# Kernel optimization log

Hardware: AMD Instinct MI355X
Metric: run time of the kernel (lower is better)

The kernel has to match this reference:

```python
import jax, jax.numpy as jnp
import numpy as np

N_IN, N_OUT = 1152, 10          # input/output capsule counts
D_IN, D_OUT = 8, 16             # input/output capsule dims
NUM_ROUTING = 3
BATCH = 256
EPS = 1e-9


def squash(s, axis=-1):
    # squash(s) = (|s|^2 / (1 + |s|^2)) * s / |s|
    sq = jnp.sum(s * s, axis=axis, keepdims=True)
    return (sq / (1.0 + sq)) * s / jnp.sqrt(sq + EPS)


def setup_inputs() -> dict:
    key = jax.random.key(0)
    kx, kw = jax.random.split(key)
    x = jax.random.normal(kx, (BATCH, D_IN, N_IN), dtype=jnp.float32)
    weight = jax.random.normal(kw, (N_IN, N_OUT, D_OUT, D_IN), dtype=jnp.float32)
    return {"x": x, "weight": weight}


def reference(x, weight):
    # u_hat[b,i,j,:] = W[i,j] @ x[b,:,i]   -> [B, N_IN, N_OUT, D_OUT]
    u_hat = jnp.einsum('ijod,bdi->bijo', weight, x)
    # routing logits b_ij shared across the batch (fully bipartite capsule graph)
    b = jnp.zeros((N_IN, N_OUT), dtype=x.dtype)
    v = None
    for _ in range(NUM_ROUTING):
        c = jax.nn.softmax(b, axis=1)                       # coupling over output caps j
        s = jnp.einsum('ij,bijo->bjo', c, u_hat)            # weighted sum of predictions
        v = squash(s)                                       # [B, N_OUT, D_OUT]
        # agreement: <u_hat, v>, averaged over batch (as in the DGL example)
        b = b + jnp.mean(jnp.einsum('bijo,bjo->bij', u_hat, v), axis=0)
    return v
```

## Files before the change

kernel.cpp:

```cpp
#include <hip/hip_runtime.h>

#define B_     256
#define NI_    1152
#define NO_    10
#define DO_    16
#define DI_    8
#define PAIRS_ 160
#define SEGS_  128
#define ISEG_  (NI_/SEGS_)
#define PP_    5
#define SC_    4


__global__ __launch_bounds__(256) void prep_kernel(const float* __restrict__ x,
                                                   float* __restrict__ xT,
                                                   float* __restrict__ blog,
                                                   float* __restrict__ cmat)
{
    int g = blockIdx.x * 256 + threadIdx.x;
    int b = g & 255;
    int r = g >> 8;
    int d = r & 7;
    int i = r >> 3;
    xT[g] = x[(size_t)b * (NI_ * DI_) + d * NI_ + i];
    if (g < NI_ * NO_) { blog[g] = 0.f; cmat[g] = 0.1f; }
}

__global__ __launch_bounds__(256) void sv_kernel(const float* __restrict__ xT,
                                                 const float* __restrict__ W,
                                                 const float* __restrict__ cmat,
                                                 float* __restrict__ partial)
{
    __shared__ __align__(16) float xs[2][DI_ * B_];
    int ps   = blockIdx.x;
    int seg  = blockIdx.y;
    int tid  = threadIdx.x;
    int lane = tid & 63;
    int pg   = __builtin_amdgcn_readfirstlane(tid >> 6);
    int p0   = ps * (4 * PP_) + pg * PP_;
    int b0   = lane * 4;
    int i0   = seg * ISEG_;

    float acc[PP_][4];
#pragma unroll
    for (int p = 0; p < PP_; ++p)
#pragma unroll
        for (int r = 0; r < 4; ++r) acc[p][r] = 0.f;

    float4 nx0, nx1;
    {
        const float4* src = (const float4*)(xT + (size_t)i0 * (DI_ * B_));
        nx0 = src[tid * 2];
        nx1 = src[tid * 2 + 1];
    }
    int buf = 0;
    for (int ii = 0; ii < ISEG_; ++ii) {
        int i = i0 + ii;
        ((float4*)xs[buf])[tid * 2]     = nx0;
        ((float4*)xs[buf])[tid * 2 + 1] = nx1;
        __syncthreads();
        if (ii + 1 < ISEG_) {
            const float4* src = (const float4*)(xT + (size_t)(i + 1) * (DI_ * B_));
            nx0 = src[tid * 2];
            nx1 = src[tid * 2 + 1];
        }
        float xv[DI_][4];
#pragma unroll
        for (int d = 0; d < DI_; ++d) {
            float4 t4 = *(const float4*)&xs[buf][d * B_ + b0];
            xv[d][0] = t4.x; xv[d][1] = t4.y; xv[d][2] = t4.z; xv[d][3] = t4.w;
        }
        const float* __restrict__ crow = cmat + i * NO_;
        const float* __restrict__ wb = W + (size_t)(i * PAIRS_ + p0) * DI_;
#pragma unroll
        for (int p = 0; p < PP_; ++p) {
            const float* wr = wb + p * DI_;
            float cv = crow[(p0 + p) >> 4];
#pragma unroll
            for (int r = 0; r < 4; ++r) {
                float u = wr[0] * xv[0][r] + wr[1] * xv[1][r]
                        + wr[2] * xv[2][r] + wr[3] * xv[3][r]
                        + wr[4] * xv[4][r] + wr[5] * xv[5][r]
                        + wr[6] * xv[6][r] + wr[7] * xv[7][r];
                acc[p][r] = fmaf(cv, u, acc[p][r]);
            }
        }
        buf ^= 1;
    }
#pragma unroll
    for (int p = 0; p < PP_; ++p) {
        float4 o4 = make_float4(acc[p][0], acc[p][1], acc[p][2], acc[p][3]);
        *(float4*)&partial[(size_t)(seg * PAIRS_ + p0 + p) * B_ + b0] = o4;
    }
}

__global__ __launch_bounds__(256) void red1_kernel(const float* __restrict__ partial,
                                                   float* __restrict__ part2)
{
    int pair = blockIdx.x;
    int sc   = blockIdx.y;
    int b    = threadIdx.x;
    float s = 0.f;
    for (int k = 0; k < SEGS_ / SC_; ++k) {
        int seg = sc * (SEGS_ / SC_) + k;
        s += partial[(size_t)(seg * PAIRS_ + pair) * B_ + b];
    }
    part2[((size_t)sc * PAIRS_ + pair) * B_ + b] = s;
}

__global__ __launch_bounds__(256) void red2_kernel(const float* __restrict__ part2,
                                                   float* __restrict__ vbuf,
                                                   float* __restrict__ out,
                                                   int write_out)
{
    int j    = blockIdx.x;
    int bq   = blockIdx.y;
    int lane = threadIdx.x & 63;
    int og   = threadIdx.x >> 6;
    int b    = bq * 64 + lane;
    __shared__ float so[DO_][64];
#pragma unroll
    for (int oo = 0; oo < 4; ++oo) {
        int o = og * 4 + oo;
        int pair = j * DO_ + o;
        float s = part2[((size_t)0 * PAIRS_ + pair) * B_ + b]
                + part2[((size_t)1 * PAIRS_ + pair) * B_ + b]
                + part2[((size_t)2 * PAIRS_ + pair) * B_ + b]
                + part2[((size_t)3 * PAIRS_ + pair) * B_ + b];
        so[o][lane] = s;
    }
    __syncthreads();
    float sq = 0.f;
#pragma unroll
    for (int o = 0; o < DO_; ++o) sq += so[o][lane] * so[o][lane];
    float f = (sq / (1.f + sq)) * rsqrtf(sq + 1e-9f);
#pragma unroll
    for (int oo = 0; oo < 4; ++oo) {
        int o = og * 4 + oo;
        float vv = so[o][lane] * f;
        vbuf[(j * DO_ + o) * B_ + b] = vv;
        if (write_out) out[(size_t)b * PAIRS_ + j * DO_ + o] = vv;
    }
}

__global__ __launch_bounds__(256) void agree_kernel(const float* __restrict__ xT,
                                                    const float* __restrict__ W,
                                                    const float* __restrict__ vbuf,
                                                    float* __restrict__ blog,
                                                    float* __restrict__ cmat)
{
    int i    = blockIdx.x;
    int lane = threadIdx.x & 63;
    int wv   = __builtin_amdgcn_readfirstlane(threadIdx.x >> 6);
    int b0   = lane * 4;

    float xv[DI_][4];
#pragma unroll
    for (int d = 0; d < DI_; ++d) {
        float4 t4 = *(const float4*)&xT[(i * DI_ + d) * B_ + b0];
        xv[d][0] = t4.x; xv[d][1] = t4.y; xv[d][2] = t4.z; xv[d][3] = t4.w;
    }
    __shared__ float js[NO_];
    __shared__ float nbs[NO_];
    for (int j = wv; j < NO_; j += 4) {
        const float* __restrict__ wj = W + (size_t)(i * NO_ + j) * DO_ * DI_;
        float aj = 0.f;
#pragma unroll
        for (int o = 0; o < DO_; ++o) {
            const float* wr = wj + o * DI_;
            float4 vv = *(const float4*)&vbuf[(j * DO_ + o) * B_ + b0];
            float u0 = wr[0]*xv[0][0] + wr[1]*xv[1][0] + wr[2]*xv[2][0] + wr[3]*xv[3][0]
                     + wr[4]*xv[4][0] + wr[5]*xv[5][0] + wr[6]*xv[6][0] + wr[7]*xv[7][0];
            float u1 = wr[0]*xv[0][1] + wr[1]*xv[1][1] + wr[2]*xv[2][1] + wr[3]*xv[3][1]
                     + wr[4]*xv[4][1] + wr[5]*xv[5][1] + wr[6]*xv[6][1] + wr[7]*xv[7][1];
            float u2 = wr[0]*xv[0][2] + wr[1]*xv[1][2] + wr[2]*xv[2][2] + wr[3]*xv[3][2]
                     + wr[4]*xv[4][2] + wr[5]*xv[5][2] + wr[6]*xv[6][2] + wr[7]*xv[7][2];
            float u3 = wr[0]*xv[0][3] + wr[1]*xv[1][3] + wr[2]*xv[2][3] + wr[3]*xv[3][3]
                     + wr[4]*xv[4][3] + wr[5]*xv[5][3] + wr[6]*xv[6][3] + wr[7]*xv[7][3];
            aj = fmaf(u0, vv.x, aj); aj = fmaf(u1, vv.y, aj);
            aj = fmaf(u2, vv.z, aj); aj = fmaf(u3, vv.w, aj);
        }
        for (int off = 32; off > 0; off >>= 1) aj += __shfl_down(aj, off);
        if (lane == 0) js[j] = aj;
    }
    __syncthreads();
    if (threadIdx.x < NO_) {
        int j = threadIdx.x;
        float nb = blog[i * NO_ + j] + js[j] * (1.f / B_);
        blog[i * NO_ + j] = nb;
        nbs[j] = nb;
    }
    __syncthreads();
    if (threadIdx.x < NO_) {
        int j = threadIdx.x;
        float m = nbs[0];
#pragma unroll
        for (int k = 1; k < NO_; ++k) m = fmaxf(m, nbs[k]);
        float ssum = 0.f;
#pragma unroll
        for (int k = 0; k < NO_; ++k) ssum += __expf(nbs[k] - m);
        cmat[i * NO_ + j] = __expf(nbs[j] - m) / ssum;
    }
}


__global__ __launch_bounds__(256) void c_old(float* __restrict__ blog,
                                             float* __restrict__ cmat, int init)
{
    int i = blockIdx.x * 256 + threadIdx.x;
    if (i >= NI_) return;
    if (init) {
#pragma unroll
        for (int j = 0; j < NO_; ++j) { cmat[i * NO_ + j] = 0.1f; blog[i * NO_ + j] = 0.f; }
        return;
    }
    float r[NO_];
    float m = -1e30f;
#pragma unroll
    for (int j = 0; j < NO_; ++j) { r[j] = blog[i * NO_ + j]; m = fmaxf(m, r[j]); }
    float s = 0.f;
#pragma unroll
    for (int j = 0; j < NO_; ++j) { r[j] = __expf(r[j] - m); s += r[j]; }
    float inv = 1.f / s;
#pragma unroll
    for (int j = 0; j < NO_; ++j) cmat[i * NO_ + j] = r[j] * inv;
}

__global__ __launch_bounds__(640) void sv_old(const float* __restrict__ x,
                                              const float* __restrict__ W,
                                              const float* __restrict__ cmat,
                                              float* __restrict__ vbuf,
                                              float* __restrict__ out,
                                              int write_out)
{
    __shared__ __align__(16) float xL[NI_ * DI_];
    __shared__ float sred[4 * PAIRS_];
    __shared__ float sfin[PAIRS_];
    int b = blockIdx.x;
    {
        const float4* xs = (const float4*)(x + (size_t)b * NI_ * DI_);
        for (int t = threadIdx.x; t < NI_ * DI_ / 4; t += 640) {
            float4 v4 = xs[t];
            int f = 4 * t;
            int d = f / NI_;
            int i = f - d * NI_;
            xL[i * DI_ + d] = v4.x; xL[(i+1) * DI_ + d] = v4.y;
            xL[(i+2) * DI_ + d] = v4.z; xL[(i+3) * DI_ + d] = v4.w;
        }
    }
    __syncthreads();
    int pair = threadIdx.x % PAIRS_;
    int seg  = threadIdx.x / PAIRS_;
    int j    = pair >> 4;
    const float4* Wq = (const float4*)W;
    float acc = 0.f;
    int i0 = seg * (NI_ / 4);
    for (int i = i0; i < i0 + NI_ / 4; ++i) {
        float4 w0 = Wq[(i * PAIRS_ + pair) * 2];
        float4 w1 = Wq[(i * PAIRS_ + pair) * 2 + 1];
        const float* xp = &xL[i * DI_];
        float u = w0.x * xp[0] + w0.y * xp[1] + w0.z * xp[2] + w0.w * xp[3]
                + w1.x * xp[4] + w1.y * xp[5] + w1.z * xp[6] + w1.w * xp[7];
        acc = fmaf(cmat[i * NO_ + j], u, acc);
    }
    sred[threadIdx.x] = acc;
    __syncthreads();
    float s = 0.f;
    if (threadIdx.x < PAIRS_) {
        s = sred[threadIdx.x] + sred[PAIRS_ + threadIdx.x]
          + sred[2 * PAIRS_ + threadIdx.x] + sred[3 * PAIRS_ + threadIdx.x];
        sfin[threadIdx.x] = s;
    }
    __syncthreads();
    if (threadIdx.x < PAIRS_) {
        int jj = threadIdx.x >> 4;
        float sq = 0.f;
#pragma unroll
        for (int o = 0; o < DO_; ++o) { float t = sfin[(jj << 4) + o]; sq = fmaf(t, t, sq); }
        float vv = s * (sq / (1.f + sq)) * rsqrtf(sq + 1e-9f);
        vbuf[b * PAIRS_ + threadIdx.x] = vv;
        if (write_out) out[b * PAIRS_ + threadIdx.x] = vv;
    }
}

__global__ __launch_bounds__(256) void agree_old(const float* __restrict__ x,
                                                 const float* __restrict__ W,
                                                 const float* __restrict__ vbuf,
                                                 float* __restrict__ blog)
{
    int i = blockIdx.x;
    int b = threadIdx.x;
    float xr[DI_];
#pragma unroll
    for (int d = 0; d < DI_; ++d) xr[d] = x[((size_t)b * DI_ + d) * NI_ + i];
    __shared__ float red[4][NO_];
    int lane = threadIdx.x & 63;
    int wv   = threadIdx.x >> 6;
    for (int j = 0; j < NO_; ++j) {
        const float* vp = &vbuf[b * PAIRS_ + j * DO_];
        float aj = 0.f;
#pragma unroll
        for (int o = 0; o < DO_; ++o) {
            const float* wr = W + (size_t)((i * NO_ + j) * DO_ + o) * DI_;
            float u = wr[0] * xr[0] + wr[1] * xr[1] + wr[2] * xr[2] + wr[3] * xr[3]
                    + wr[4] * xr[4] + wr[5] * xr[5] + wr[6] * xr[6] + wr[7] * xr[7];
            aj = fmaf(u, vp[o], aj);
        }
        float val = aj;
        for (int off = 32; off > 0; off >>= 1) val += __shfl_down(val, off);
        if (lane == 0) red[wv][j] = val;
    }
    __syncthreads();
    if (threadIdx.x < NO_) {
        float sum = red[0][threadIdx.x] + red[1][threadIdx.x]
                  + red[2][threadIdx.x] + red[3][threadIdx.x];
        blog[i * NO_ + threadIdx.x] += sum * (1.f / B_);
    }
}


extern "C" void kernel_launch(void* const* d_in, const int* in_sizes, int n_in,
                              void* d_out, int out_size, void* d_ws, size_t ws_size,
                              hipStream_t stream)
{
    const float* x = (const float*)d_in[0];
    const float* W = (const float*)d_in[1];
    float* out = (float*)d_out;

    const size_t XT_N  = (size_t)NI_ * DI_ * B_;
    const size_t LOG_N = NI_ * NO_;
    const size_t V_N   = PAIRS_ * B_;
    const size_t P_N   = (size_t)SEGS_ * PAIRS_ * B_;
    const size_t P2_N  = (size_t)SC_ * PAIRS_ * B_;
    const size_t NEED  = (XT_N + 2 * LOG_N + V_N + P_N + P2_N) * sizeof(float);

    if (ws_size >= NEED) {
        float* xT      = (float*)d_ws;
        float* blog    = xT + XT_N;
        float* cmat    = blog + LOG_N;
        float* vbuf    = cmat + LOG_N;
        float* partial = vbuf + V_N;
        float* part2   = partial + P_N;

        prep_kernel<<<(NI_ * DI_ * B_) / 256, 256, 0, stream>>>(x, xT, blog, cmat);
        for (int it = 0; it < 3; ++it) {
            sv_kernel<<<dim3(8, SEGS_), 256, 0, stream>>>(xT, W, cmat, partial);
            red1_kernel<<<dim3(PAIRS_, SC_), 256, 0, stream>>>(partial, part2);
            red2_kernel<<<dim3(NO_, B_ / 64), 256, 0, stream>>>(part2, vbuf, out,
                                                                it == 2 ? 1 : 0);
            if (it < 2) agree_kernel<<<NI_, 256, 0, stream>>>(xT, W, vbuf, blog, cmat);
        }
    } else {
        float* blog = (float*)d_ws;
        float* cmat = blog + LOG_N;
        float* vbuf = cmat + LOG_N;
        for (int it = 0; it < 3; ++it) {
            c_old<<<(NI_ + 255) / 256, 256, 0, stream>>>(blog, cmat, it == 0 ? 1 : 0);
            sv_old<<<B_, 640, 0, stream>>>(x, W, cmat, vbuf, out, it == 2 ? 1 : 0);
            if (it < 2) agree_old<<<NI_, 256, 0, stream>>>(x, W, vbuf, blog);
        }
    }
}
```

Before: 188.7 us.

## Tile the x transpose, register-stream x in sv, fuse two-stage reduction

The prep kernel now transposes x through a padded 64x64 shared-memory tile, so both the reads and the writes are coalesced, and the logit/coupling init moves to extra blocks. sv_kernel drops its shared double buffer and __syncthreads, loading each thread's x values straight from global memory into registers with a one-step prefetch, and adds a min-blocks launch bound. The two reduction kernels become one that sums all 128 segments per element before squashing, which removes a launch and the intermediate buffer. In exchange the single reduction runs far fewer blocks and has longer serial loops, and register pressure in sv rises.

Result: faster. 184.9 us (-2.0%).

```diff
diff --git a/kernel.cpp b/kernel.cpp
--- a/kernel.cpp
+++ b/kernel.cpp
@@ -9,7 +9,6 @@
 #define SEGS_  128
 #define ISEG_  (NI_/SEGS_)
 #define PP_    5
-#define SC_    4
 
 
 __global__ __launch_bounds__(256) void prep_kernel(const float* __restrict__ x,
@@ -17,27 +16,40 @@
                                                    float* __restrict__ blog,
                                                    float* __restrict__ cmat)
 {
-    int g = blockIdx.x * 256 + threadIdx.x;
-    int b = g & 255;
-    int r = g >> 8;
-    int d = r & 7;
-    int i = r >> 3;
-    xT[g] = x[(size_t)b * (NI_ * DI_) + d * NI_ + i];
-    if (g < NI_ * NO_) { blog[g] = 0.f; cmat[g] = 0.1f; }
-}
-
-__global__ __launch_bounds__(256) void sv_kernel(const float* __restrict__ xT,
-                                                 const float* __restrict__ W,
-                                                 const float* __restrict__ cmat,
-                                                 float* __restrict__ partial)
-{
-    __shared__ __align__(16) float xs[2][DI_ * B_];
+    int vb = blockIdx.x;
+    int tid = threadIdx.x, lane = tid & 63, wv = tid >> 6;
+    if (vb < 576) {
+        __shared__ float tile[64 * 65];
+        int d = vb & 7, rest = vb >> 3, tb = rest & 3, ti = rest >> 2;
+        int i0 = ti * 64, b0 = tb * 64;
+#pragma unroll
+        for (int k = 0; k < 16; ++k) {
+            int bL = wv * 16 + k;
+            tile[bL * 65 + lane] = x[(size_t)(b0 + bL) * (NI_ * DI_) + d * NI_ + i0 + lane];
+        }
+        __syncthreads();
+#pragma unroll
+        for (int k = 0; k < 16; ++k) {
+            int iL = wv * 16 + k;
+            xT[((size_t)(i0 + iL) * DI_ + d) * B_ + b0 + lane] = tile[lane * 65 + iL];
+        }
+    } else {
+        int g = (vb - 576) * 256 + tid;
+        if (g < NI_ * NO_) { blog[g] = 0.f; cmat[g] = 0.1f; }
+    }
+}
+
+__global__ __launch_bounds__(256, 4) void sv_kernel(const float* __restrict__ xT,
+                                                    const float* __restrict__ W,
+                                                    const float* __restrict__ cmat,
+                                                    float* __restrict__ partial)
+{
     int ps   = blockIdx.x;
     int seg  = blockIdx.y;
     int tid  = threadIdx.x;
     int lane = tid & 63;
-    int pg   = __builtin_amdgcn_readfirstlane(tid >> 6);
-    int p0   = ps * (4 * PP_) + pg * PP_;
+    int wv   = __builtin_amdgcn_readfirstlane(tid >> 6);
+    int p0   = ps * (4 * PP_) + wv * PP_;
     int b0   = lane * 4;
     int i0   = seg * ISEG_;
 
@@ -47,100 +59,74 @@
 #pragma unroll
         for (int r = 0; r < 4; ++r) acc[p][r] = 0.f;
 
-    float4 nx0, nx1;
-    {
-        const float4* src = (const float4*)(xT + (size_t)i0 * (DI_ * B_));
-        nx0 = src[tid * 2];
-        nx1 = src[tid * 2 + 1];
-    }
-    int buf = 0;
+    float4 nx[DI_];
+#pragma unroll
+    for (int d = 0; d < DI_; ++d)
+        nx[d] = *(const float4*)&xT[((size_t)i0 * DI_ + d) * B_ + b0];
+
     for (int ii = 0; ii < ISEG_; ++ii) {
         int i = i0 + ii;
-        ((float4*)xs[buf])[tid * 2]     = nx0;
-        ((float4*)xs[buf])[tid * 2 + 1] = nx1;
-        __syncthreads();
+        float4 cx[DI_];
+#pragma unroll
+        for (int d = 0; d < DI_; ++d) cx[d] = nx[d];
         if (ii + 1 < ISEG_) {
-            const float4* src = (const float4*)(xT + (size_t)(i + 1) * (DI_ * B_));
-            nx0 = src[tid * 2];
-            nx1 = src[tid * 2 + 1];
-        }
-        float xv[DI_][4];
-#pragma unroll
-        for (int d = 0; d < DI_; ++d) {
-            float4 t4 = *(const float4*)&xs[buf][d * B_ + b0];
-            xv[d][0] = t4.x; xv[d][1] = t4.y; xv[d][2] = t4.z; xv[d][3] = t4.w;
+#pragma unroll
+            for (int d = 0; d < DI_; ++d)
+                nx[d] = *(const float4*)&xT[((size_t)(i + 1) * DI_ + d) * B_ + b0];
         }
         const float* __restrict__ crow = cmat + i * NO_;
-        const float* __restrict__ wb = W + (size_t)(i * PAIRS_ + p0) * DI_;
+        const float* __restrict__ wb   = W + (size_t)(i * PAIRS_ + p0) * DI_;
 #pragma unroll
         for (int p = 0; p < PP_; ++p) {
             const float* wr = wb + p * DI_;
             float cv = crow[(p0 + p) >> 4];
-#pragma unroll
-            for (int r = 0; r < 4; ++r) {
-                float u = wr[0] * xv[0][r] + wr[1] * xv[1][r]
-                        + wr[2] * xv[2][r] + wr[3] * xv[3][r]
-                        + wr[4] * xv[4][r] + wr[5] * xv[5][r]
-                        + wr[6] * xv[6][r] + wr[7] * xv[7][r];
-                acc[p][r] = fmaf(cv, u, acc[p][r]);
+            float u0 = wr[0] * cx[0].x, u1 = wr[0] * cx[0].y;
+            float u2 = wr[0] * cx[0].z, u3 = wr[0] * cx[0].w;
+#pragma unroll
+            for (int d = 1; d < DI_; ++d) {
+                u0 = fmaf(wr[d], (&cx[d].x)[0], u0);
+                u1 = fmaf(wr[d], (&cx[d].x)[1], u1);
+                u2 = fmaf(wr[d], (&cx[d].x)[2], u2);
+                u3 = fmaf(wr[d], (&cx[d].x)[3], u3);
             }
-        }
-        buf ^= 1;
-    }
-#pragma unroll
-    for (int p = 0; p < PP_; ++p) {
-        float4 o4 = make_float4(acc[p][0], acc[p][1], acc[p][2], acc[p][3]);
-        *(float4*)&partial[(size_t)(seg * PAIRS_ + p0 + p) * B_ + b0] = o4;
-    }
-}
-
-__global__ __launch_bounds__(256) void red1_kernel(const float* __restrict__ partial,
-                                                   float* __restrict__ part2)
-{
-    int pair = blockIdx.x;
-    int sc   = blockIdx.y;
-    int b    = threadIdx.x;
+            acc[p][0] = fmaf(cv, u0, acc[p][0]);
+            acc[p][1] = fmaf(cv, u1, acc[p][1]);
+            acc[p][2] = fmaf(cv, u2, acc[p][2]);
+            acc[p][3] = fmaf(cv, u3, acc[p][3]);
+        }
+    }
+#pragma unroll
+    for (int p = 0; p < PP_; ++p)
+        *(float4*)&partial[(size_t)(seg * PAIRS_ + p0 + p) * B_ + b0] =
+            make_float4(acc[p][0], acc[p][1], acc[p][2], acc[p][3]);
+}
+
+__global__ __launch_bounds__(256) void red_kernel(const float* __restrict__ partial,
+                                                  float* __restrict__ vbuf,
+                                                  float* __restrict__ out,
+                                                  int write_out)
+{
+    int j   = blockIdx.x;
+    int bc  = blockIdx.y;
+    int o   = threadIdx.x >> 4;
+    int b_l = threadIdx.x & 15;
+    int b   = bc * 16 + b_l;
+    int pair = j * DO_ + o;
+
     float s = 0.f;
-    for (int k = 0; k < SEGS_ / SC_; ++k) {
-        int seg = sc * (SEGS_ / SC_) + k;
+    for (int seg = 0; seg < SEGS_; ++seg)
         s += partial[(size_t)(seg * PAIRS_ + pair) * B_ + b];
-    }
-    part2[((size_t)sc * PAIRS_ + pair) * B_ + b] = s;
-}
-
-__global__ __launch_bounds__(256) void red2_kernel(const float* __restrict__ part2,
-                                                   float* __restrict__ vbuf,
-                                                   float* __restrict__ out,
-                                                   int write_out)
-{
-    int j    = blockIdx.x;
-    int bq   = blockIdx.y;
-    int lane = threadIdx.x & 63;
-    int og   = threadIdx.x >> 6;
-    int b    = bq * 64 + lane;
-    __shared__ float so[DO_][64];
-#pragma unroll
-    for (int oo = 0; oo < 4; ++oo) {
-        int o = og * 4 + oo;
-        int pair = j * DO_ + o;
-        float s = part2[((size_t)0 * PAIRS_ + pair) * B_ + b]
-                + part2[((size_t)1 * PAIRS_ + pair) * B_ + b]
-                + part2[((size_t)2 * PAIRS_ + pair) * B_ + b]
-                + part2[((size_t)3 * PAIRS_ + pair) * B_ + b];
-        so[o][lane] = s;
-    }
+
+    __shared__ float so[DO_][17];
+    so[o][b_l] = s;
     __syncthreads();
     float sq = 0.f;
 #pragma unroll
-    for (int o = 0; o < DO_; ++o) sq += so[o][lane] * so[o][lane];
+    for (int oo = 0; oo < DO_; ++oo) { float t = so[oo][b_l]; sq = fmaf(t, t, sq); }
     float f = (sq / (1.f + sq)) * rsqrtf(sq + 1e-9f);
-#pragma unroll
-    for (int oo = 0; oo < 4; ++oo) {
-        int o = og * 4 + oo;
-        float vv = so[o][lane] * f;
-        vbuf[(j * DO_ + o) * B_ + b] = vv;
-        if (write_out) out[(size_t)b * PAIRS_ + j * DO_ + o] = vv;
-    }
+    float vv = s * f;
+    vbuf[pair * B_ + b] = vv;
+    if (write_out) out[(size_t)b * PAIRS_ + pair] = vv;
 }
 
 __global__ __launch_bounds__(256) void agree_kernel(const float* __restrict__ xT,
@@ -157,7 +143,7 @@
     float xv[DI_][4];
 #pragma unroll
     for (int d = 0; d < DI_; ++d) {
-        float4 t4 = *(const float4*)&xT[(i * DI_ + d) * B_ + b0];
+        float4 t4 = *(const float4*)&xT[((size_t)i * DI_ + d) * B_ + b0];
         xv[d][0] = t4.x; xv[d][1] = t4.y; xv[d][2] = t4.z; xv[d][3] = t4.w;
     }
     __shared__ float js[NO_];
@@ -168,38 +154,35 @@
 #pragma unroll
         for (int o = 0; o < DO_; ++o) {
             const float* wr = wj + o * DI_;
-            float4 vv = *(const float4*)&vbuf[(j * DO_ + o) * B_ + b0];
-            float u0 = wr[0]*xv[0][0] + wr[1]*xv[1][0] + wr[2]*xv[2][0] + wr[3]*xv[3][0]
-                     + wr[4]*xv[4][0] + wr[5]*xv[5][0] + wr[6]*xv[6][0] + wr[7]*xv[7][0];
-            float u1 = wr[0]*xv[0][1] + wr[1]*xv[1][1] + wr[2]*xv[2][1] + wr[3]*xv[3][1]
-                     + wr[4]*xv[4][1] + wr[5]*xv[5][1] + wr[6]*xv[6][1] + wr[7]*xv[7][1];
-            float u2 = wr[0]*xv[0][2] + wr[1]*xv[1][2] + wr[2]*xv[2][2] + wr[3]*xv[3][2]
-                     + wr[4]*xv[4][2] + wr[5]*xv[5][2] + wr[6]*xv[6][2] + wr[7]*xv[7][2];
-            float u3 = wr[0]*xv[0][3] + wr[1]*xv[1][3] + wr[2]*xv[2][3] + wr[3]*xv[3][3]
-                     + wr[4]*xv[4][3] + wr[5]*xv[5][3] + wr[6]*xv[6][3] + wr[7]*xv[7][3];
-            aj = fmaf(u0, vv.x, aj); aj = fmaf(u1, vv.y, aj);
-            aj = fmaf(u2, vv.z, aj); aj = fmaf(u3, vv.w, aj);
+            float4 vv4 = *(const float4*)&vbuf[(j * DO_ + o) * B_ + b0];
+            float u0 = wr[0] * xv[0][0], u1 = wr[0] * xv[0][1];
+            float u2 = wr[0] * xv[0][2], u3 = wr[0] * xv[0][3];
+#pragma unroll
+            for (int d = 1; d < DI_; ++d) {
+                u0 = fmaf(wr[d], xv[d][0], u0); u1 = fmaf(wr[d], xv[d][1], u1);
+                u2 = fmaf(wr[d], xv[d][2], u2); u3 = fmaf(wr[d], xv[d][3], u3);
+            }
+            aj = fmaf(u0, vv4.x, aj); aj = fmaf(u1, vv4.y, aj);
+            aj = fmaf(u2, vv4.z, aj); aj = fmaf(u3, vv4.w, aj);
         }
         for (int off = 32; off > 0; off >>= 1) aj += __shfl_down(aj, off);
         if (lane == 0) js[j] = aj;
     }
     __syncthreads();
     if (threadIdx.x < NO_) {
-        int j = threadIdx.x;
-        float nb = blog[i * NO_ + j] + js[j] * (1.f / B_);
-        blog[i * NO_ + j] = nb;
-        nbs[j] = nb;
+        float nb = blog[i * NO_ + threadIdx.x] + js[threadIdx.x] * (1.f / B_);
+        blog[i * NO_ + threadIdx.x] = nb;
+        nbs[threadIdx.x] = nb;
     }
     __syncthreads();
     if (threadIdx.x < NO_) {
-        int j = threadIdx.x;
         float m = nbs[0];
 #pragma unroll
         for (int k = 1; k < NO_; ++k) m = fmaxf(m, nbs[k]);
         float ssum = 0.f;
 #pragma unroll
         for (int k = 0; k < NO_; ++k) ssum += __expf(nbs[k] - m);
-        cmat[i * NO_ + j] = __expf(nbs[j] - m) / ssum;
+        cmat[i * NO_ + threadIdx.x] = __expf(nbs[threadIdx.x] - m) / ssum;
     }
 }
 
@@ -214,8 +197,7 @@
         for (int j = 0; j < NO_; ++j) { cmat[i * NO_ + j] = 0.1f; blog[i * NO_ + j] = 0.f; }
         return;
     }
-    float r[NO_];
-    float m = -1e30f;
+    float r[NO_]; float m = -1e30f;
 #pragma unroll
     for (int j = 0; j < NO_; ++j) { r[j] = blog[i * NO_ + j]; m = fmaxf(m, r[j]); }
     float s = 0.f;
@@ -230,8 +212,7 @@
                                               const float* __restrict__ W,
                                               const float* __restrict__ cmat,
                                               float* __restrict__ vbuf,
-                                              float* __restrict__ out,
-                                              int write_out)
+                                              float* __restrict__ out, int write_out)
 {
     __shared__ __align__(16) float xL[NI_ * DI_];
     __shared__ float sred[4 * PAIRS_];
@@ -241,9 +222,7 @@
         const float4* xs = (const float4*)(x + (size_t)b * NI_ * DI_);
         for (int t = threadIdx.x; t < NI_ * DI_ / 4; t += 640) {
             float4 v4 = xs[t];
-            int f = 4 * t;
-            int d = f / NI_;
-            int i = f - d * NI_;
+            int f = 4 * t; int d = f / NI_; int i = f - d * NI_;
             xL[i * DI_ + d] = v4.x; xL[(i+1) * DI_ + d] = v4.y;
             xL[(i+2) * DI_ + d] = v4.z; xL[(i+3) * DI_ + d] = v4.w;
         }
@@ -331,8 +310,7 @@
     const size_t LOG_N = NI_ * NO_;
     const size_t V_N   = PAIRS_ * B_;
     const size_t P_N   = (size_t)SEGS_ * PAIRS_ * B_;
-    const size_t P2_N  = (size_t)SC_ * PAIRS_ * B_;
-    const size_t NEED  = (XT_N + 2 * LOG_N + V_N + P_N + P2_N) * sizeof(float);
+    const size_t NEED  = (XT_N + 2 * LOG_N + V_N + P_N) * sizeof(float);
 
     if (ws_size >= NEED) {
         float* xT      = (float*)d_ws;
@@ -340,14 +318,12 @@
         float* cmat    = blog + LOG_N;
         float* vbuf    = cmat + LOG_N;
         float* partial = vbuf + V_N;
-        float* part2   = partial + P_N;
-
-        prep_kernel<<<(NI_ * DI_ * B_) / 256, 256, 0, stream>>>(x, xT, blog, cmat);
+
+        prep_kernel<<<576 + 45, 256, 0, stream>>>(x, xT, blog, cmat);
         for (int it = 0; it < 3; ++it) {
             sv_kernel<<<dim3(8, SEGS_), 256, 0, stream>>>(xT, W, cmat, partial);
-            red1_kernel<<<dim3(PAIRS_, SC_), 256, 0, stream>>>(partial, part2);
-            red2_kernel<<<dim3(NO_, B_ / 64), 256, 0, stream>>>(part2, vbuf, out,
-                                                                it == 2 ? 1 : 0);
+            red_kernel<<<dim3(NO_, B_ / 16), 256, 0, stream>>>(partial, vbuf, out,
+                                                               it == 2 ? 1 : 0);
             if (it < 2) agree_kernel<<<NI_, 256, 0, stream>>>(xT, W, vbuf, blog, cmat);
         }
     } else {
```
